# Kernel tuning notes

Measured on AMD Instinct MI355X. Metric: run time of the kernel, lower is better.

Reference implementation:

```python
import jax, jax.numpy as jnp
import numpy as np
from jax import lax

HEADS = 8
DIM_HEAD = 64
DIM = HEADS * DIM_HEAD  # 512


def _dwconv(x_nchw, w):
    # depthwise 3x3, stride 1, pad 1 (SAME), groups = channels
    return lax.conv_general_dilated(
        x_nchw, w, window_strides=(1, 1), padding='SAME',
        feature_group_count=x_nchw.shape[1],
        dimension_numbers=('NCHW', 'OIHW', 'NCHW'))


def setup_inputs() -> dict:
    key = jax.random.key(0)
    ks = jax.random.split(key, 9)
    b, h, w, c = 4, 256, 256, DIM
    s = 1.0 / np.sqrt(c)
    return {
        'x_in':    jax.random.normal(ks[0], (b, h, w, c), jnp.float32),
        'Wq':      jax.random.normal(ks[1], (c, DIM), jnp.float32) * s,
        'Wk':      jax.random.normal(ks[2], (c, DIM), jnp.float32) * s,
        'Wv':      jax.random.normal(ks[3], (c, DIM), jnp.float32) * s,
        'rescale': jnp.ones((HEADS, 1, 1), jnp.float32),
        'proj_w':  jax.random.normal(ks[4], (DIM, c), jnp.float32) * s,
        'proj_b':  jnp.zeros((c,), jnp.float32),
        'conv1_w': jax.random.normal(ks[5], (c, 1, 3, 3), jnp.float32) * (1.0 / 3.0),
        'conv2_w': jax.random.normal(ks[6], (c, 1, 3, 3), jnp.float32) * (1.0 / 3.0),
    }


def reference(x_in, Wq, Wk, Wv, rescale, proj_w, proj_b, conv1_w, conv2_w):
    b, h, w, c = x_in.shape
    n = h * w
    x = x_in.reshape(b, n, c)
    q_inp = x @ Wq  # [b, n, heads*d]
    k_inp = x @ Wk
    v_inp = x @ Wv

    def heads_dn(t):  # [b, n, heads*d] -> [b, heads, d, n]
        return t.reshape(b, n, HEADS, DIM_HEAD).transpose(0, 2, 3, 1)

    q = heads_dn(q_inp)
    k = heads_dn(k_inp)
    v = heads_dn(v_inp)

    # L2-normalize along token axis (F.normalize, eps=1e-12)
    qn = q / jnp.maximum(jnp.linalg.norm(q, axis=-1, keepdims=True), 1e-12)
    kn = k / jnp.maximum(jnp.linalg.norm(k, axis=-1, keepdims=True), 1e-12)

    # channel attention: [b, heads, d, d]
    attn = jnp.einsum('bhdn,bhen->bhde', kn, qn) * rescale
    attn = jax.nn.softmax(attn, axis=-1)
    xo = jnp.einsum('bhde,bhen->bhdn', attn, v)  # [b, heads, d, n]

    xo = xo.transpose(0, 3, 1, 2).reshape(b, n, HEADS * DIM_HEAD)
    out_c = (xo @ proj_w + proj_b).reshape(b, h, w, c)

    # depthwise conv positional embedding on v_inp
    vp = v_inp.reshape(b, h, w, c).transpose(0, 3, 1, 2)  # NCHW
    vp = _dwconv(vp, conv1_w)
    vp = jax.nn.gelu(vp, approximate=False)
    vp = _dwconv(vp, conv2_w)
    out_p = vp.transpose(0, 2, 3, 1)

    return out_c + out_p
```

## Files before the change

### kernel.cpp

```cpp
#include <hip/hip_runtime.h>
#include <math.h>

typedef unsigned short u16;
typedef unsigned int   u32;
typedef __attribute__((ext_vector_type(4))) float f32x4;
typedef __attribute__((ext_vector_type(8))) short bf16x8;
typedef __attribute__((ext_vector_type(8))) u16   u16x8;
typedef __attribute__((ext_vector_type(4))) u16   u16x4;

#define DEVI static __device__ __forceinline__

DEVI float bf2f(u16 a){ u32 u=((u32)a)<<16; float f; __builtin_memcpy(&f,&u,4); return f; }
DEVI u16 f2bf(float f){ u32 u; __builtin_memcpy(&u,&f,4); u=u+0x7fffu+((u>>16)&1u); return (u16)(u>>16); }

DEVI void gload16(const u16* src, u16* lds){
  __builtin_amdgcn_global_load_lds((const __attribute__((address_space(1))) u32*)src,
                                   (__attribute__((address_space(3))) u32*)lds, 16, 0, 0);
}

__global__ void k_wvt(const float* __restrict__ Wv, u16* __restrict__ WvT){
  int n = blockIdx.x;
  for (int k = threadIdx.x; k < 512; k += 256)
    WvT[(size_t)n*512 + k] = f2bf(Wv[(size_t)k*512 + n]);
}
__global__ void k_wrep(const float* __restrict__ w1, const float* __restrict__ w2, float* __restrict__ wt){
  int s = blockIdx.x/9, tap = blockIdx.x%9, c = threadIdx.x;
  const float* w = s ? w2 : w1;
  wt[(size_t)(s*9+tap)*512 + c] = w[(size_t)c*9 + tap];
}

__global__ __launch_bounds__(1024, 4) void k_gemm_v(const float* __restrict__ x, const u16* __restrict__ WvT,
                                                    u16* __restrict__ v, u16* __restrict__ xbT){
  __shared__ __align__(16) u16 Al[128*64];
  __shared__ __align__(16) u16 Bl[512*64];
  const int tid = threadIdx.x;
  const int l = tid & 63, w = tid >> 6;
  const int wr = w >> 3, wc = w & 7;
  const long r0 = (long)blockIdx.x * 128;
  f32x4 acc[4][4] = {};
  for (int k0 = 0; k0 < 512; k0 += 64){
    {
      int row = tid >> 3, c = tid & 7;
      const float* xp = x + (r0 + row)*512 + k0 + c*8;
      f32x4 va = *(const f32x4*)xp, vb = *(const f32x4*)(xp+4);
      u16x8 o;
      o[0]=f2bf(va.x); o[1]=f2bf(va.y); o[2]=f2bf(va.z); o[3]=f2bf(va.w);
      o[4]=f2bf(vb.x); o[5]=f2bf(vb.y); o[6]=f2bf(vb.z); o[7]=f2bf(vb.w);
      *(u16x8*)&Al[row*64 + ((c ^ (row&7))*8)] = o;
    }
    #pragma unroll
    for (int i = 0; i < 4; ++i){
      int blkrow = w*32 + i*8;
      int r = blkrow + (l>>3);
      const u16* src = WvT + (size_t)r*512 + k0 + (((l&7) ^ ((l>>3)&7))*8);
      gload16(src, &Bl[blkrow*64]);
    }
    __syncthreads();
    #pragma unroll
    for (int ks = 0; ks < 2; ++ks){
      bf16x8 af[4], bfr[4];
      #pragma unroll
      for (int mf = 0; mf < 4; ++mf){
        int row = wr*64 + mf*16 + (l&15);
        af[mf] = *(const bf16x8*)&Al[row*64 + (((ks*4 + (l>>4)) ^ (row&7))*8)];
      }
      #pragma unroll
      for (int nf = 0; nf < 4; ++nf){
        int row = wc*64 + nf*16 + (l&15);
        bfr[nf] = *(const bf16x8*)&Bl[row*64 + (((ks*4 + (l>>4)) ^ (row&7))*8)];
      }
      #pragma unroll
      for (int mf = 0; mf < 4; ++mf)
        #pragma unroll
        for (int nf = 0; nf < 4; ++nf)
          acc[mf][nf] = __builtin_amdgcn_mfma_f32_16x16x32_bf16(af[mf], bfr[nf], acc[mf][nf], 0,0,0);
    }
    {
      int chloc = tid & 63, tg = tid >> 6;
      u16x8 o;
      #pragma unroll
      for (int j = 0; j < 8; ++j){
        int tok = tg*8 + j;
        o[j] = Al[tok*64 + (((chloc>>3) ^ (tok&7))*8) + (chloc&7)];
      }
      *(u16x8*)(xbT + (size_t)(k0 + chloc)*262144 + r0 + tg*8) = o;
    }
    __syncthreads();
  }
  #pragma unroll
  for (int mf = 0; mf < 4; ++mf)
    #pragma unroll
    for (int nf = 0; nf < 4; ++nf){
      int col = wc*64 + nf*16 + (l&15);
      #pragma unroll
      for (int j = 0; j < 4; ++j){
        long row = r0 + wr*64 + mf*16 + (l>>4)*4 + j;
        v[(size_t)row*512 + col] = f2bf(acc[mf][nf][j]);
      }
    }
}

__global__ __launch_bounds__(1024, 4) void k_syrk(const u16* __restrict__ xbT, float* __restrict__ P){
  __shared__ __align__(16) u16 AL[256*64];
  __shared__ __align__(16) u16 BL[256*64];
  const int bid = blockIdx.x;
  const int cs = bid & 63, combo = (bid>>6)%3, b = bid/192;
  const int hA = (combo==2) ? 1 : 0;
  const int tid = threadIdx.x;
  const int l = tid & 63, w = tid>>6, wi = w>>2, wj = w&3;
  const long tokb0 = (long)b*65536 + (long)cs*1024;
  const u16* Bread = (combo==1) ? BL : AL;
  f32x4 acc[4][4] = {};
  for (int st = 0; st < 16; ++st){
    const long tokb = tokb0 + st*64;
    #pragma unroll
    for (int i = 0; i < 2; ++i){
      int blkrow = w*16 + i*8;
      int r = blkrow + (l>>3);
      const u16* src = xbT + (size_t)(hA*256 + r)*262144 + tokb + (((l&7) ^ ((l>>3)&7))*8);
      gload16(src, &AL[blkrow*64]);
    }
    if (combo == 1){
      #pragma unroll
      for (int i = 0; i < 2; ++i){
        int blkrow = w*16 + i*8;
        int r = blkrow + (l>>3);
        const u16* src = xbT + (size_t)(256 + r)*262144 + tokb + (((l&7) ^ ((l>>3)&7))*8);
        gload16(src, &BL[blkrow*64]);
      }
    }
    __syncthreads();
    #pragma unroll
    for (int ks = 0; ks < 2; ++ks){
      bf16x8 af[4], bfr[4];
      #pragma unroll
      for (int mf = 0; mf < 4; ++mf){
        int row = wi*64 + mf*16 + (l&15);
        af[mf] = *(const bf16x8*)&AL[row*64 + (((ks*4 + (l>>4)) ^ (row&7))*8)];
      }
      #pragma unroll
      for (int nf = 0; nf < 4; ++nf){
        int row = wj*64 + nf*16 + (l&15);
        bfr[nf] = *(const bf16x8*)&Bread[row*64 + (((ks*4 + (l>>4)) ^ (row&7))*8)];
      }
      #pragma unroll
      for (int mf = 0; mf < 4; ++mf)
        #pragma unroll
        for (int nf = 0; nf < 4; ++nf)
          acc[mf][nf] = __builtin_amdgcn_mfma_f32_16x16x32_bf16(af[mf], bfr[nf], acc[mf][nf], 0,0,0);
    }
    __syncthreads();
  }
  float* Pb = P + (size_t)bid*65536;
  #pragma unroll
  for (int mf = 0; mf < 4; ++mf)
    #pragma unroll
    for (int nf = 0; nf < 4; ++nf)
      #pragma unroll
      for (int j = 0; j < 4; ++j){
        int il = wi*64 + mf*16 + (l>>4)*4 + j;
        int jl = wj*64 + nf*16 + (l&15);
        Pb[il*256 + jl] = acc[mf][nf][j];
      }
}

__global__ void k_sred(const float* __restrict__ P, float* __restrict__ S){
  int bid = blockIdx.x;
  int il = bid & 255, combo = (bid>>8)%3, b = bid/768;
  int hi = (combo==2)?1:0, hj = (combo==0)?0:1;
  int jl = threadIdx.x;
  float s = 0.f;
  for (int cs = 0; cs < 64; ++cs)
    s += P[((size_t)(b*192 + combo*64 + cs))*65536 + il*256 + jl];
  int I = hi*256 + il, J = hj*256 + jl;
  S[((size_t)b*512 + I)*512 + J] = s;
  if (combo == 1) S[((size_t)b*512 + J)*512 + I] = s;
}

__global__ __launch_bounds__(256) void k_a1(const float* __restrict__ S, const float* __restrict__ Wq,
                                            const float* __restrict__ Wk, float* __restrict__ T, float* __restrict__ U){
  int bid = blockIdx.x;
  int b = bid>>6, rem = bid&63, which = rem>>5, rbase = (rem&31)*16;
  const float* W = which ? Wk : Wq;
  float* O = which ? U : T;
  int tid = threadIdx.x;
  int rg = tid>>6, c0 = (tid&63)*8;
  const float* Sr = S + (size_t)b*262144 + (size_t)(rbase + rg*4)*512;
  float acc[4][8] = {};
  for (int k = 0; k < 512; ++k){
    float s0 = Sr[k], s1 = Sr[512+k], s2 = Sr[1024+k], s3 = Sr[1536+k];
    f32x4 wa = *(const f32x4*)(W + (size_t)k*512 + c0);
    f32x4 wb = *(const f32x4*)(W + (size_t)k*512 + c0 + 4);
    #pragma unroll
    for (int j = 0; j < 4; ++j){
      acc[0][j]   += s0*wa[j]; acc[1][j]   += s1*wa[j]; acc[2][j]   += s2*wa[j]; acc[3][j]   += s3*wa[j];
      acc[0][4+j] += s0*wb[j]; acc[1][4+j] += s1*wb[j]; acc[2][4+j] += s2*wb[j]; acc[3][4+j] += s3*wb[j];
    }
  }
  float* Ob = O + (size_t)b*262144;
  #pragma unroll
  for (int i = 0; i < 4; ++i){
    f32x4 o0, o1;
    o0.x=acc[i][0]; o0.y=acc[i][1]; o0.z=acc[i][2]; o0.w=acc[i][3];
    o1.x=acc[i][4]; o1.y=acc[i][5]; o1.z=acc[i][6]; o1.w=acc[i][7];
    *(f32x4*)(Ob + (size_t)(rbase+rg*4+i)*512 + c0)     = o0;
    *(f32x4*)(Ob + (size_t)(rbase+rg*4+i)*512 + c0 + 4) = o1;
  }
}

__global__ void k_a2(const float* __restrict__ Wq, const float* __restrict__ Wk,
                     const float* __restrict__ T, const float* __restrict__ U,
                     float* __restrict__ G, float* __restrict__ q2, float* __restrict__ k2){
  int b = blockIdx.x>>3, h = blockIdx.x&7;
  int tid = threadIdx.x;
  int d0 = (tid>>4)*4, e0 = (tid&15)*4;
  const float* Tb = T + (size_t)b*262144;
  float acc[4][4] = {};
  for (int i = 0; i < 512; ++i){
    f32x4 wk = *(const f32x4*)(Wk + (size_t)i*512 + h*64 + d0);
    f32x4 tv = *(const f32x4*)(Tb + (size_t)i*512 + h*64 + e0);
    #pragma unroll
    for (int di = 0; di < 4; ++di)
      #pragma unroll
      for (int ej = 0; ej < 4; ++ej) acc[di][ej] += wk[di]*tv[ej];
  }
  float* Gb = G + ((size_t)(b*8+h))*4096;
  #pragma unroll
  for (int di = 0; di < 4; ++di)
    #pragma unroll
    for (int ej = 0; ej < 4; ++ej) Gb[(d0+di)*64 + e0+ej] = acc[di][ej];
  if (tid < 64){
    int e = tid; float a = 0.f;
    for (int j = 0; j < 512; ++j) a += Wq[(size_t)j*512 + h*64 + e] * Tb[(size_t)j*512 + h*64 + e];
    q2[b*512 + h*64 + e] = a;
  } else if (tid < 128){
    int d = tid - 64; float a = 0.f;
    const float* Ub = U + (size_t)b*262144;
    for (int j = 0; j < 512; ++j) a += Wk[(size_t)j*512 + h*64 + d] * Ub[(size_t)j*512 + h*64 + d];
    k2[b*512 + h*64 + d] = a;
  }
}

__global__ void k_a3(const float* __restrict__ G, const float* __restrict__ resc,
                     const float* __restrict__ q2, const float* __restrict__ k2, float* __restrict__ Aa){
  int b = blockIdx.x>>3, h = blockIdx.x&7;
  int d = threadIdx.x;
  const float* g = G + ((size_t)(b*8+h))*4096 + d*64;
  float kn = fmaxf(sqrtf(k2[b*512 + h*64 + d]), 1e-12f);
  float sc = resc[h] / kn;
  float m = -3.4e38f;
  for (int e = 0; e < 64; ++e){
    float qn = fmaxf(sqrtf(q2[b*512 + h*64 + e]), 1e-12f);
    m = fmaxf(m, g[e]*sc/qn);
  }
  float ssum = 0.f;
  for (int e = 0; e < 64; ++e){
    float qn = fmaxf(sqrtf(q2[b*512 + h*64 + e]), 1e-12f);
    ssum += expf(g[e]*sc/qn - m);
  }
  float inv = 1.0f/ssum;
  float* ao = Aa + ((size_t)(b*8+h))*4096 + d*64;
  for (int e = 0; e < 64; ++e){
    float qn = fmaxf(sqrtf(q2[b*512 + h*64 + e]), 1e-12f);
    ao[e] = expf(g[e]*sc/qn - m)*inv;
  }
}

__global__ void k_a4(const float* __restrict__ Aa, const float* __restrict__ pw, u16* __restrict__ MT){
  int bid = blockIdx.x;
  int jt = bid&3, h = (bid>>2)&7, b = bid>>5;
  int tid = threadIdx.x;
  int j = jt*128 + (tid&127), eh = tid>>7;
  const float* Ab = Aa + ((size_t)(b*8+h))*4096;
  float acc[32] = {};
  for (int d = 0; d < 64; ++d){
    float p = pw[(size_t)(h*64+d)*512 + j];
    const float* ar = Ab + d*64 + eh*32;
    #pragma unroll
    for (int q = 0; q < 8; ++q){
      f32x4 pa = *(const f32x4*)(ar + q*4);
      acc[q*4+0] += pa.x*p; acc[q*4+1] += pa.y*p; acc[q*4+2] += pa.z*p; acc[q*4+3] += pa.w*p;
    }
  }
  u16* mo = MT + (size_t)b*262144 + (size_t)j*512 + h*64 + eh*32;
  #pragma unroll
  for (int q = 0; q < 16; ++q){
    u32 pk = (u32)f2bf(acc[2*q]) | ((u32)f2bf(acc[2*q+1])<<16);
    *(u32*)&mo[2*q] = pk;
  }
}

__global__ __launch_bounds__(256) void k_conv_fused(const u16* __restrict__ v, const float* __restrict__ wt,
                                                    u16* __restrict__ cbuf){
  __shared__ float vtf[400*16];
  __shared__ float t1f[324*16];
  const int bid = blockIdx.x;
  const int g = bid & 31, tx = (bid>>5)&15, ty = (bid>>9)&15, b = bid>>13;
  const int c0 = g*16, oy0 = ty*16, ox0 = tx*16;
  const int tid = threadIdx.x;
  const int quad = tid & 3;

  for (int k = 0; k < 7; ++k){
    int q = tid + k*256; if (q >= 1600) break;
    int pos = q >> 2;
    int ly = pos / 20, lx = pos - ly*20;
    int gy = oy0 - 2 + ly, gx = ox0 - 2 + lx;
    f32x4 val = {};
    if (gy >= 0 && gy < 256 && gx >= 0 && gx < 256){
      u16x4 raw = *(const u16x4*)(v + ((size_t)(b*65536 + gy*256 + gx))*512 + c0 + quad*4);
      val.x = bf2f(raw[0]); val.y = bf2f(raw[1]); val.z = bf2f(raw[2]); val.w = bf2f(raw[3]);
    }
    *(f32x4*)&vtf[pos*16 + quad*4] = val;
  }

  f32x4 wq[9];
  #pragma unroll
  for (int tap = 0; tap < 9; ++tap)
    wq[tap] = *(const f32x4*)(wt + (size_t)tap*512 + c0 + quad*4);
  __syncthreads();

  for (int k = 0; k < 6; ++k){
    int q = tid + k*256; if (q >= 1296) break;
    int pos = q >> 2;
    int y1 = pos / 18, x1 = pos - y1*18;
    int gy1 = oy0 - 1 + y1, gx1 = ox0 - 1 + x1;
    bool inimg = (gy1 >= 0 && gy1 < 256 && gx1 >= 0 && gx1 < 256);
    const float* base = &vtf[(y1*20 + x1)*16 + quad*4];
    float acc[4] = {};
    #pragma unroll
    for (int tap = 0; tap < 9; ++tap){
      int dy = tap/3, dx = tap - dy*3;
      f32x4 vv = *(const f32x4*)(base + (dy*20 + dx)*16);
      #pragma unroll
      for (int j = 0; j < 4; ++j) acc[j] += vv[j]*wq[tap][j];
    }
    f32x4 o;
    #pragma unroll
    for (int j = 0; j < 4; ++j){
      float a = acc[j];
      float gl = a / (1.0f + __expf(-1.5957691216f*a*(1.0f + 0.044715f*a*a)));
      o[j] = inimg ? gl : 0.0f;
    }
    *(f32x4*)&t1f[pos*16 + quad*4] = o;
  }

  #pragma unroll
  for (int tap = 0; tap < 9; ++tap)
    wq[tap] = *(const f32x4*)(wt + (size_t)(9+tap)*512 + c0 + quad*4);
  __syncthreads();

  #pragma unroll
  for (int k = 0; k < 4; ++k){
    int q = tid + k*256;
    int pos = q >> 2;
    int y2 = pos >> 4, x2 = pos & 15;
    const float* base = &t1f[(y2*18 + x2)*16 + quad*4];
    float acc[4] = {};
    #pragma unroll
    for (int tap = 0; tap < 9; ++tap){
      int dy = tap/3, dx = tap - dy*3;
      f32x4 tt = *(const f32x4*)(base + (dy*18 + dx)*16);
      #pragma unroll
      for (int j = 0; j < 4; ++j) acc[j] += tt[j]*wq[tap][j];
    }
    u16x4 o;
    #pragma unroll
    for (int j = 0; j < 4; ++j) o[j] = f2bf(acc[j]);
    size_t tok = (size_t)b*65536 + (size_t)(oy0+y2)*256 + (ox0+x2);
    *(u16x4*)(cbuf + tok*512 + c0 + quad*4) = o;
  }
}

__global__ __launch_bounds__(512) void k_gemm_out(const u16* __restrict__ v, const u16* __restrict__ MT,
                                                  const float* __restrict__ proj_b, const u16* __restrict__ cbuf,
                                                  float* __restrict__ out){
  __shared__ __align__(16) u16 Al[2][128*64];
  __shared__ __align__(16) u16 Bl[2][256*64];
  const int tid = threadIdx.x;
  const int l = tid & 63, w = tid >> 6;
  const int wr = w >> 2, wc = w & 3;
  const int bid = blockIdx.x;
  const int wg = (bid & 7)*512 + (bid >> 3);
  const long r0 = (long)(wg >> 1) * 128;
  const int  c0b = (wg & 1) * 256;
  const int  b = (int)(r0 >> 16);
  const u16* Mb = MT + (size_t)b*262144;
  f32x4 acc[4][4] = {};

  auto STAGE = [&](int buf, int k0){
    #pragma unroll
    for (int i = 0; i < 2; ++i){
      int blkrow = w*16 + i*8;
      int r = blkrow + (l>>3);
      const u16* src = v + (size_t)(r0 + r)*512 + k0 + (((l&7) ^ (r&7))*8);
      gload16(src, &Al[buf][blkrow*64]);
    }
    #pragma unroll
    for (int i = 0; i < 4; ++i){
      int blkrow = w*32 + i*8;
      int r = blkrow + (l>>3);
      const u16* src = Mb + (size_t)(c0b + r)*512 + k0 + (((l&7) ^ (r&7))*8);
      gload16(src, &Bl[buf][blkrow*64]);
    }
  };

  STAGE(0, 0);
  __syncthreads();
  for (int t = 0; t < 8; ++t){
    const int cur = t & 1;
    if (t < 7) STAGE(cur^1, (t+1)*64);
    #pragma unroll
    for (int ks = 0; ks < 2; ++ks){
      bf16x8 af[4], bfr[4];
      #pragma unroll
      for (int mf = 0; mf < 4; ++mf){
        int row = wr*64 + mf*16 + (l&15);
        af[mf] = *(const bf16x8*)&Al[cur][row*64 + (((ks*4 + (l>>4)) ^ (row&7))*8)];
      }
      #pragma unroll
      for (int nf = 0; nf < 4; ++nf){
        int row = wc*64 + nf*16 + (l&15);
        bfr[nf] = *(const bf16x8*)&Bl[cur][row*64 + (((ks*4 + (l>>4)) ^ (row&7))*8)];
      }
      #pragma unroll
      for (int mf = 0; mf < 4; ++mf)
        #pragma unroll
        for (int nf = 0; nf < 4; ++nf)
          acc[mf][nf] = __builtin_amdgcn_mfma_f32_16x16x32_bf16(af[mf], bfr[nf], acc[mf][nf], 0,0,0);
    }
    __syncthreads();
  }
  #pragma unroll
  for (int mf = 0; mf < 4; ++mf)
    #pragma unroll
    for (int nf = 0; nf < 4; ++nf){
      int col = c0b + wc*64 + nf*16 + (l&15);
      float pb = proj_b[col];
      #pragma unroll
      for (int j = 0; j < 4; ++j){
        long row = r0 + wr*64 + mf*16 + (l>>4)*4 + j;
        out[(size_t)row*512 + col] = acc[mf][nf][j] + pb + bf2f(cbuf[(size_t)row*512 + col]);
      }
    }
}

extern "C" void kernel_launch(void* const* d_in, const int* in_sizes, int n_in,
                              void* d_out, int out_size, void* d_ws, size_t ws_size,
                              hipStream_t stream){
  const float* x   = (const float*)d_in[0];
  const float* Wq  = (const float*)d_in[1];
  const float* Wk  = (const float*)d_in[2];
  const float* Wv  = (const float*)d_in[3];
  const float* rsc = (const float*)d_in[4];
  const float* pw  = (const float*)d_in[5];
  const float* pb  = (const float*)d_in[6];
  const float* w1  = (const float*)d_in[7];
  const float* w2  = (const float*)d_in[8];
  float* out = (float*)d_out;
  char* ws = (char*)d_ws;

  const size_t MB256 = 268435456;
  u16*   v    = (u16*)ws;
  u16*   xbT  = (u16*)(ws + MB256);
  u16*   cbuf = xbT;
  char*  sm0  = ws + 2*MB256;
  float* P    = (float*)d_out;

  float* S   = (float*)(sm0);
  float* Tm  = (float*)(sm0 + 4194304);
  float* Um  = (float*)(sm0 + 8388608);
  float* G   = (float*)(sm0 + 12582912);
  float* Aa  = (float*)(sm0 + 13107200);
  float* q2  = (float*)(sm0 + 13631488);
  float* k2  = (float*)(sm0 + 13639680);
  u16*   MT  = (u16*)  (sm0 + 13647872);
  u16*   WvT = (u16*)  (sm0 + 15745024);
  float* wt  = (float*)(sm0 + 16269312);

  k_wvt <<<512, 256, 0, stream>>>(Wv, WvT);
  k_wrep<<<18, 512, 0, stream>>>(w1, w2, wt);
  k_gemm_v<<<2048, 1024, 0, stream>>>(x, WvT, v, xbT);
  k_syrk<<<768, 1024, 0, stream>>>(xbT, P);
  k_sred<<<3072, 256, 0, stream>>>(P, S);
  k_a1<<<256, 256, 0, stream>>>(S, Wq, Wk, Tm, Um);
  k_a2<<<32, 256, 0, stream>>>(Wq, Wk, Tm, Um, G, q2, k2);
  k_a3<<<32, 64, 0, stream>>>(G, rsc, q2, k2, Aa);
  k_a4<<<128, 256, 0, stream>>>(Aa, pw, MT);
  k_conv_fused<<<32768, 256, 0, stream>>>(v, wt, cbuf);
  k_gemm_out<<<4096, 512, 0, stream>>>(v, MT, pb, cbuf, out);
}
```

Measured before the change: 1.627 ms.

## Register-block depthwise convs, pad LDS rows, remap conv blocks, prefetch x in gemm_v

Each thread in the fused depthwise conv kernel now computes four horizontally adjacent outputs. It reuses a sliding window of LDS loads across taps, which cuts the LDS reads per output. The LDS row stride is padded from 16 to 20 floats to reduce bank conflicts, and the block index is remapped so that consecutive blocks are spread differently across XCDs. In the V projection GEMM, the next fp32 x tile is loaded into registers before the current one is used. This adds register pressure and some redundant edge computation in the first conv stage.

```diff
diff --git a/kernel.cpp b/kernel.cpp
--- a/kernel.cpp
+++ b/kernel.cpp
@@ -38,15 +38,19 @@
   const int wr = w >> 3, wc = w & 7;
   const long r0 = (long)blockIdx.x * 128;
   f32x4 acc[4][4] = {};
+  const int arow = tid >> 3, ac = tid & 7;
+  const float* xp = x + (r0 + arow)*512 + ac*8;
+  f32x4 va = *(const f32x4*)xp, vb = *(const f32x4*)(xp+4);
   for (int k0 = 0; k0 < 512; k0 += 64){
     {
-      int row = tid >> 3, c = tid & 7;
-      const float* xp = x + (r0 + row)*512 + k0 + c*8;
-      f32x4 va = *(const f32x4*)xp, vb = *(const f32x4*)(xp+4);
       u16x8 o;
       o[0]=f2bf(va.x); o[1]=f2bf(va.y); o[2]=f2bf(va.z); o[3]=f2bf(va.w);
       o[4]=f2bf(vb.x); o[5]=f2bf(vb.y); o[6]=f2bf(vb.z); o[7]=f2bf(vb.w);
-      *(u16x8*)&Al[row*64 + ((c ^ (row&7))*8)] = o;
+      *(u16x8*)&Al[arow*64 + ((ac ^ (arow&7))*8)] = o;
+    }
+    if (k0 < 448){
+      va = *(const f32x4*)(xp + k0 + 64);
+      vb = *(const f32x4*)(xp + k0 + 68);
     }
     #pragma unroll
     for (int i = 0; i < 4; ++i){
@@ -292,10 +296,10 @@
 
 __global__ __launch_bounds__(256) void k_conv_fused(const u16* __restrict__ v, const float* __restrict__ wt,
                                                     u16* __restrict__ cbuf){
-  __shared__ float vtf[400*16];
-  __shared__ float t1f[324*16];
-  const int bid = blockIdx.x;
-  const int g = bid & 31, tx = (bid>>5)&15, ty = (bid>>9)&15, b = bid>>13;
+  __shared__ float vtf[400*20];
+  __shared__ float t1f[324*20];
+  const int logical = (blockIdx.x & 7)*4096 + (blockIdx.x >> 3);
+  const int g = logical & 31, tx = (logical>>5)&15, ty = (logical>>9)&15, b = logical>>13;
   const int c0 = g*16, oy0 = ty*16, ox0 = tx*16;
   const int tid = threadIdx.x;
   const int quad = tid & 3;
@@ -310,7 +314,7 @@
       u16x4 raw = *(const u16x4*)(v + ((size_t)(b*65536 + gy*256 + gx))*512 + c0 + quad*4);
       val.x = bf2f(raw[0]); val.y = bf2f(raw[1]); val.z = bf2f(raw[2]); val.w = bf2f(raw[3]);
     }
-    *(f32x4*)&vtf[pos*16 + quad*4] = val;
+    *(f32x4*)&vtf[pos*20 + quad*4] = val;
   }
 
   f32x4 wq[9];
@@ -319,29 +323,47 @@
     wq[tap] = *(const f32x4*)(wt + (size_t)tap*512 + c0 + quad*4);
   __syncthreads();
 
-  for (int k = 0; k < 6; ++k){
-    int q = tid + k*256; if (q >= 1296) break;
-    int pos = q >> 2;
-    int y1 = pos / 18, x1 = pos - y1*18;
-    int gy1 = oy0 - 1 + y1, gx1 = ox0 - 1 + x1;
-    bool inimg = (gy1 >= 0 && gy1 < 256 && gx1 >= 0 && gx1 < 256);
-    const float* base = &vtf[(y1*20 + x1)*16 + quad*4];
-    float acc[4] = {};
-    #pragma unroll
-    for (int tap = 0; tap < 9; ++tap){
-      int dy = tap/3, dx = tap - dy*3;
-      f32x4 vv = *(const f32x4*)(base + (dy*20 + dx)*16);
-      #pragma unroll
-      for (int j = 0; j < 4; ++j) acc[j] += vv[j]*wq[tap][j];
-    }
-    f32x4 o;
-    #pragma unroll
-    for (int j = 0; j < 4; ++j){
-      float a = acc[j];
-      float gl = a / (1.0f + __expf(-1.5957691216f*a*(1.0f + 0.044715f*a*a)));
-      o[j] = inimg ? gl : 0.0f;
-    }
-    *(f32x4*)&t1f[pos*16 + quad*4] = o;
+  for (int task = tid; task < 1440; task += 256){
+    int tq = task & 3;
+    int rest = task >> 2;
+    if (rest >= 90) break;
+    int chunk = rest % 5, y1 = rest / 5;
+    int x1b = chunk*4;
+    float acc[4][4] = {{0.f}};
+    #pragma unroll
+    for (int cc = 0; cc < 6; ++cc){
+      int lx = x1b + cc; lx = lx > 19 ? 19 : lx;
+      #pragma unroll
+      for (int dy = 0; dy < 3; ++dy){
+        f32x4 s = *(const f32x4*)&vtf[((y1+dy)*20 + lx)*20 + tq*4];
+        #pragma unroll
+        for (int ox = 0; ox < 4; ++ox){
+          int dx = cc - ox;
+          if (dx >= 0 && dx < 3){
+            f32x4 w = wq[dy*3 + dx];
+            #pragma unroll
+            for (int j = 0; j < 4; ++j) acc[ox][j] += s[j]*w[j];
+          }
+        }
+      }
+    }
+    int gy1 = oy0 - 1 + y1;
+    #pragma unroll
+    for (int ox = 0; ox < 4; ++ox){
+      int x1 = x1b + ox;
+      if (x1 < 18){
+        int gx1 = ox0 - 1 + x1;
+        bool inimg = (gy1 >= 0 && gy1 < 256 && gx1 >= 0 && gx1 < 256);
+        f32x4 o;
+        #pragma unroll
+        for (int j = 0; j < 4; ++j){
+          float a = acc[ox][j];
+          float gl = a / (1.0f + __expf(-1.5957691216f*a*(1.0f + 0.044715f*a*a)));
+          o[j] = inimg ? gl : 0.0f;
+        }
+        *(f32x4*)&t1f[(y1*18 + x1)*20 + tq*4] = o;
+      }
+    }
   }
 
   #pragma unroll
@@ -349,25 +371,36 @@
     wq[tap] = *(const f32x4*)(wt + (size_t)(9+tap)*512 + c0 + quad*4);
   __syncthreads();
 
-  #pragma unroll
-  for (int k = 0; k < 4; ++k){
-    int q = tid + k*256;
-    int pos = q >> 2;
-    int y2 = pos >> 4, x2 = pos & 15;
-    const float* base = &t1f[(y2*18 + x2)*16 + quad*4];
-    float acc[4] = {};
-    #pragma unroll
-    for (int tap = 0; tap < 9; ++tap){
-      int dy = tap/3, dx = tap - dy*3;
-      f32x4 tt = *(const f32x4*)(base + (dy*18 + dx)*16);
-      #pragma unroll
-      for (int j = 0; j < 4; ++j) acc[j] += tt[j]*wq[tap][j];
-    }
-    u16x4 o;
-    #pragma unroll
-    for (int j = 0; j < 4; ++j) o[j] = f2bf(acc[j]);
-    size_t tok = (size_t)b*65536 + (size_t)(oy0+y2)*256 + (ox0+x2);
-    *(u16x4*)(cbuf + tok*512 + c0 + quad*4) = o;
+  {
+    int rest = tid >> 2;
+    int chunk = rest & 3, y2 = rest >> 2;
+    int x2b = chunk*4;
+    float acc[4][4] = {{0.f}};
+    #pragma unroll
+    for (int cc = 0; cc < 6; ++cc){
+      int lx = x2b + cc;
+      #pragma unroll
+      for (int dy = 0; dy < 3; ++dy){
+        f32x4 s = *(const f32x4*)&t1f[((y2+dy)*18 + lx)*20 + quad*4];
+        #pragma unroll
+        for (int ox = 0; ox < 4; ++ox){
+          int dx = cc - ox;
+          if (dx >= 0 && dx < 3){
+            f32x4 w = wq[dy*3 + dx];
+            #pragma unroll
+            for (int j = 0; j < 4; ++j) acc[ox][j] += s[j]*w[j];
+          }
+        }
+      }
+    }
+    #pragma unroll
+    for (int ox = 0; ox < 4; ++ox){
+      u16x4 o;
+      #pragma unroll
+      for (int j = 0; j < 4; ++j) o[j] = f2bf(acc[ox][j]);
+      size_t tok = (size_t)b*65536 + (size_t)(oy0+y2)*256 + (ox0 + x2b + ox);
+      *(u16x4*)(cbuf + tok*512 + c0 + quad*4) = o;
+    }
   }
 }
 
```

New measurement: 1.751 ms. +7.6%, slower.

## Enlarge output GEMM tile, prefetch x in V GEMM, swizzle conv blocks

Applied to the files above, without the earlier changes.

The output projection GEMM moves from a 128x256 to a 256x256 tile per block, with 8x4 MFMA fragments per wave and double-buffered dynamic LDS. This halves the block count and improves operand reuse. The V projection GEMM now loads the next x tile into registers before the current tile's compute, to hide global load latency. The conv kernel's block index is remapped so that blocks sharing a channel group and location spread across the XCDs. The larger tile raises LDS use to 128KB and register pressure, which limits occupancy.

```diff
diff --git a/kernel.cpp b/kernel.cpp
--- a/kernel.cpp
+++ b/kernel.cpp
@@ -38,15 +38,19 @@
   const int wr = w >> 3, wc = w & 7;
   const long r0 = (long)blockIdx.x * 128;
   f32x4 acc[4][4] = {};
+  const int arow = tid >> 3, ac = tid & 7;
+  const float* xp = x + (r0 + arow)*512 + ac*8;
+  f32x4 va = *(const f32x4*)xp, vb = *(const f32x4*)(xp+4);
   for (int k0 = 0; k0 < 512; k0 += 64){
     {
-      int row = tid >> 3, c = tid & 7;
-      const float* xp = x + (r0 + row)*512 + k0 + c*8;
-      f32x4 va = *(const f32x4*)xp, vb = *(const f32x4*)(xp+4);
       u16x8 o;
       o[0]=f2bf(va.x); o[1]=f2bf(va.y); o[2]=f2bf(va.z); o[3]=f2bf(va.w);
       o[4]=f2bf(vb.x); o[5]=f2bf(vb.y); o[6]=f2bf(vb.z); o[7]=f2bf(vb.w);
-      *(u16x8*)&Al[row*64 + ((c ^ (row&7))*8)] = o;
+      *(u16x8*)&Al[arow*64 + ((ac ^ (arow&7))*8)] = o;
+    }
+    if (k0 < 448){
+      va = *(const f32x4*)(xp + k0 + 64);
+      vb = *(const f32x4*)(xp + k0 + 68);
     }
     #pragma unroll
     for (int i = 0; i < 4; ++i){
@@ -294,8 +298,8 @@
                                                     u16* __restrict__ cbuf){
   __shared__ float vtf[400*16];
   __shared__ float t1f[324*16];
-  const int bid = blockIdx.x;
-  const int g = bid & 31, tx = (bid>>5)&15, ty = (bid>>9)&15, b = bid>>13;
+  const int logical = (blockIdx.x & 7)*4096 + (blockIdx.x >> 3);
+  const int g = logical & 31, tx = (logical>>5)&15, ty = (logical>>9)&15, b = logical>>13;
   const int c0 = g*16, oy0 = ty*16, ox0 = tx*16;
   const int tid = threadIdx.x;
   const int quad = tid & 3;
@@ -371,36 +375,35 @@
   }
 }
 
-__global__ __launch_bounds__(512) void k_gemm_out(const u16* __restrict__ v, const u16* __restrict__ MT,
-                                                  const float* __restrict__ proj_b, const u16* __restrict__ cbuf,
-                                                  float* __restrict__ out){
-  __shared__ __align__(16) u16 Al[2][128*64];
-  __shared__ __align__(16) u16 Bl[2][256*64];
+__global__ __launch_bounds__(512, 2) void k_gemm_out(const u16* __restrict__ v, const u16* __restrict__ MT,
+                                                     const float* __restrict__ proj_b, const u16* __restrict__ cbuf,
+                                                     float* __restrict__ out){
+  extern __shared__ __align__(16) u16 sm[];
   const int tid = threadIdx.x;
   const int l = tid & 63, w = tid >> 6;
   const int wr = w >> 2, wc = w & 3;
   const int bid = blockIdx.x;
-  const int wg = (bid & 7)*512 + (bid >> 3);
-  const long r0 = (long)(wg >> 1) * 128;
+  const int wg = (bid & 7)*256 + (bid >> 3);
+  const long r0 = (long)(wg >> 1) * 256;
   const int  c0b = (wg & 1) * 256;
   const int  b = (int)(r0 >> 16);
   const u16* Mb = MT + (size_t)b*262144;
-  f32x4 acc[4][4] = {};
+  f32x4 acc[8][4] = {};
 
   auto STAGE = [&](int buf, int k0){
-    #pragma unroll
-    for (int i = 0; i < 2; ++i){
-      int blkrow = w*16 + i*8;
-      int r = blkrow + (l>>3);
-      const u16* src = v + (size_t)(r0 + r)*512 + k0 + (((l&7) ^ (r&7))*8);
-      gload16(src, &Al[buf][blkrow*64]);
-    }
+    u16* Ab = sm + buf*16384;
+    u16* Bb = sm + 32768 + buf*16384;
     #pragma unroll
     for (int i = 0; i < 4; ++i){
       int blkrow = w*32 + i*8;
       int r = blkrow + (l>>3);
-      const u16* src = Mb + (size_t)(c0b + r)*512 + k0 + (((l&7) ^ (r&7))*8);
-      gload16(src, &Bl[buf][blkrow*64]);
+      gload16(v + (size_t)(r0 + r)*512 + k0 + (((l&7) ^ (r&7))*8), Ab + blkrow*64);
+    }
+    #pragma unroll
+    for (int i = 0; i < 4; ++i){
+      int blkrow = w*32 + i*8;
+      int r = blkrow + (l>>3);
+      gload16(Mb + (size_t)(c0b + r)*512 + k0 + (((l&7) ^ (r&7))*8), Bb + blkrow*64);
     }
   };
 
@@ -409,36 +412,36 @@
   for (int t = 0; t < 8; ++t){
     const int cur = t & 1;
     if (t < 7) STAGE(cur^1, (t+1)*64);
+    const u16* Al = sm + cur*16384;
+    const u16* Bl = sm + 32768 + cur*16384;
     #pragma unroll
     for (int ks = 0; ks < 2; ++ks){
-      bf16x8 af[4], bfr[4];
-      #pragma unroll
-      for (int mf = 0; mf < 4; ++mf){
-        int row = wr*64 + mf*16 + (l&15);
-        af[mf] = *(const bf16x8*)&Al[cur][row*64 + (((ks*4 + (l>>4)) ^ (row&7))*8)];
-      }
+      bf16x8 bfr[4];
       #pragma unroll
       for (int nf = 0; nf < 4; ++nf){
         int row = wc*64 + nf*16 + (l&15);
-        bfr[nf] = *(const bf16x8*)&Bl[cur][row*64 + (((ks*4 + (l>>4)) ^ (row&7))*8)];
-      }
-      #pragma unroll
-      for (int mf = 0; mf < 4; ++mf)
+        bfr[nf] = *(const bf16x8*)&Bl[row*64 + (((ks*4 + (l>>4)) ^ (row&7))*8)];
+      }
+      #pragma unroll
+      for (int mf = 0; mf < 8; ++mf){
+        int row = wr*128 + mf*16 + (l&15);
+        bf16x8 af = *(const bf16x8*)&Al[row*64 + (((ks*4 + (l>>4)) ^ (row&7))*8)];
         #pragma unroll
         for (int nf = 0; nf < 4; ++nf)
-          acc[mf][nf] = __builtin_amdgcn_mfma_f32_16x16x32_bf16(af[mf], bfr[nf], acc[mf][nf], 0,0,0);
+          acc[mf][nf] = __builtin_amdgcn_mfma_f32_16x16x32_bf16(af, bfr[nf], acc[mf][nf], 0,0,0);
+      }
     }
     __syncthreads();
   }
   #pragma unroll
-  for (int mf = 0; mf < 4; ++mf)
+  for (int mf = 0; mf < 8; ++mf)
     #pragma unroll
     for (int nf = 0; nf < 4; ++nf){
       int col = c0b + wc*64 + nf*16 + (l&15);
       float pb = proj_b[col];
       #pragma unroll
       for (int j = 0; j < 4; ++j){
-        long row = r0 + wr*64 + mf*16 + (l>>4)*4 + j;
+        long row = r0 + wr*128 + mf*16 + (l>>4)*4 + j;
         out[(size_t)row*512 + col] = acc[mf][nf][j] + pb + bf2f(cbuf[(size_t)row*512 + col]);
       }
     }
@@ -487,5 +490,5 @@
   k_a3<<<32, 64, 0, stream>>>(G, rsc, q2, k2, Aa);
   k_a4<<<128, 256, 0, stream>>>(Aa, pw, MT);
   k_conv_fused<<<32768, 256, 0, stream>>>(v, wt, cbuf);
-  k_gemm_out<<<4096, 512, 0, stream>>>(v, MT, pb, cbuf, out);
-}
+  k_gemm_out<<<2048, 512, 131072, stream>>>(v, MT, pb, cbuf, out);
+}
```

After: 1.536 ms. -5.6%, faster.
